# Kernel tuning notes

Hardware: AMD Instinct MI355X
Metric: run time of the kernel (lower is better)

The kernel has to match this reference:

```python
import jax, jax.numpy as jnp
import numpy as np

H = 8        # heads
R = 8        # rank of Lambda
WWIN = 8     # topk window w
T = 2        # num_iterations


def _rotate_half(x):
    h = x.shape[-1] // 2
    return jnp.concatenate([-x[..., h:], x[..., :h]], axis=-1)


def _gelu(x):
    return jax.nn.gelu(x, approximate=False)  # torch nn.GELU default is exact erf


def _forward(target, context, Wt, bt, Wc, bc, Ws1, bs1, Ws2, bs2,
             Wa1, ba1, Wa2, ba2, Wl1, bl1, Wl2, bl2, step_sizes, Wo, bo):
    B, L, D = target.shape
    K = context.shape[1]
    HD = D // H
    u = (target @ Wt + bt).reshape(B, L, H, HD).transpose(0, 2, 1, 3)   # [B,H,L,HD]
    v = (context @ Wc + bc).reshape(B, K, H, HD).transpose(0, 2, 1, 3)  # [B,H,K,HD]

    # scored-window connectivity: first scorer layer is separable over concat([t_i, c_j])
    h1 = (target @ Ws1[:D])[:, :, None, :] + (context @ Ws1[D:])[:, None, :, :] + bs1  # [B,L,K,EH]
    scores = (_gelu(h1) @ Ws2 + bs2)[..., 0]                                           # [B,L,K]
    _, idx = jax.lax.top_k(scores, WWIN)                                               # [B,L,w]
    E = L * WWIN
    edge_j = idx.reshape(B, E)
    edge_i = jnp.broadcast_to(jnp.repeat(jnp.arange(L), WWIN)[None], (B, E))

    # per-edge learnable params R_ij = alpha_ij I + Lambda_ij Lambda_ij^T
    tf = jnp.take_along_axis(target, edge_i[..., None], axis=1)   # [B,E,D]
    cf = jnp.take_along_axis(context, edge_j[..., None], axis=1)  # [B,E,D]
    ef = jnp.concatenate([tf, cf], axis=-1)                       # [B,E,2D]
    alphas = jax.nn.softplus(_gelu(ef @ Wa1 + ba1) @ Wa2 + ba2)[..., 0]     # [B,E]
    Lam = (_gelu(ef @ Wl1 + bl1) @ Wl2 + bl2).reshape(B, E, H, R, HD)
    Lam = Lam / jnp.maximum(jnp.linalg.norm(Lam, axis=-1, keepdims=True), 1e-12)

    # relative-position rotary applied to gathered target states (model_type='SC')
    inv_freq = 1.0 / (10000.0 ** (jnp.arange(0, HD, 2, dtype=jnp.float32) / HD))
    ang = (edge_i - edge_j).astype(jnp.float32)[..., None] * inv_freq       # [B,E,HD/2]
    cos = jnp.concatenate([jnp.cos(ang), jnp.cos(ang)], -1)[:, None]        # [B,1,E,HD]
    sin = jnp.concatenate([jnp.sin(ang), jnp.sin(ang)], -1)[:, None]

    def scatter_edges(res_b, ei_b):  # res_b [H,E,HD] -> [H,L,HD]
        return jax.ops.segment_sum(res_b.transpose(1, 0, 2), ei_b,
                                   num_segments=L).transpose(1, 0, 2)

    for t in range(T):
        step = jax.nn.softplus(step_sizes[t])[None, None, :, None]          # [1,1,L,1] (max_len == L)
        u_i = jnp.take_along_axis(u, edge_i[:, None, :, None], axis=2)      # [B,H,E,HD]
        u_i = u_i * cos + _rotate_half(u_i) * sin
        v_j = jnp.take_along_axis(v, edge_j[:, None, :, None], axis=2)      # [B,H,E,HD]
        diff = u_i - v_j
        Ld = jnp.einsum('behrd,bhed->bher', Lam, diff)                      # [B,H,E,R]
        residual = alphas[:, None, :, None] * diff + jnp.einsum('bher,behrd->bhed', Ld, Lam)
        u = u - step * jax.vmap(scatter_edges)(residual, edge_i)

    y = u.transpose(0, 2, 1, 3).reshape(B, L, D) @ Wo + bo  # dropout is identity in eval
    return y


def setup_inputs() -> dict:
    key = jax.random.key(0)
    B, L, K, D, EH = 2, 2048, 2048, 512, 16
    HD = D // H
    ks = iter(jax.random.split(key, 24))

    def lin(i, o):
        return jax.random.normal(next(ks), (i, o), jnp.float32) * (1.0 / float(np.sqrt(i)))

    def bias(o):
        return jnp.zeros((o,), jnp.float32)

    return {
        'target': jax.random.normal(next(ks), (B, L, D), jnp.float32),
        'context': jax.random.normal(next(ks), (B, K, D), jnp.float32),
        'Wt': lin(D, D), 'bt': bias(D),
        'Wc': lin(D, D), 'bc': bias(D),
        'Ws1': lin(2 * D, EH), 'bs1': bias(EH),
        'Ws2': lin(EH, 1), 'bs2': bias(1),
        'Wa1': lin(2 * D, EH), 'ba1': bias(EH),
        'Wa2': lin(EH, 1), 'ba2': bias(1),
        'Wl1': lin(2 * D, EH), 'bl1': bias(EH),
        'Wl2': lin(EH, H * R * HD), 'bl2': bias(H * R * HD),
        'step_sizes': jnp.full((T, L), -2.2, jnp.float32),
        'Wo': lin(D, D), 'bo': bias(D),
    }


def reference(target, context, Wt, bt, Wc, bc, Ws1, bs1, Ws2, bs2,
              Wa1, ba1, Wa2, ba2, Wl1, bl1, Wl2, bl2, step_sizes, Wo, bo):
    return _forward(target, context, Wt, bt, Wc, bc, Ws1, bs1, Ws2, bs2,
                    Wa1, ba1, Wa2, ba2, Wl1, bl1, Wl2, bl2, step_sizes, Wo, bo)
```

## Files before the change

kernel.cpp:

```cpp
#include <hip/hip_runtime.h>
#include <math.h>

#define BB 2
#define LL 2048
#define KK 2048
#define DD 512
#define HH 8
#define HD_ 64
#define RR 8
#define WWIN 8
#define NE (LL * WWIN)

typedef __attribute__((ext_vector_type(8))) short bf16x8s;
typedef __attribute__((ext_vector_type(4))) float f32x4;

__device__ __forceinline__ float gelu_f(float x) {
    return 0.5f * x * (1.0f + erff(x * 0.70710678118654752f));
}
__device__ __forceinline__ float softplus_f(float x) {
    return (x > 20.0f) ? x : log1pf(expf(x));
}
__device__ __forceinline__ unsigned short f2bf(float f) {
    unsigned int x = __float_as_uint(f);
    x += 0x7FFFu + ((x >> 16) & 1u);
    return (unsigned short)(x >> 16);
}
__device__ __forceinline__ float bf2f(unsigned short s) {
    return __uint_as_float(((unsigned int)s) << 16);
}

__device__ __forceinline__ void gemm_bf16_body(
    const float* __restrict__ A, const float* __restrict__ W,
    const float* __restrict__ bias, float* __restrict__ C,
    int M, int N, int Kd, int bx, int by) {
    __shared__ short As[128][40];
    __shared__ short Bs[64][40];
    const int tid = threadIdx.x;
    const int m0 = bx * 128, n0 = by * 64;
    const int wv = tid >> 6, lane = tid & 63;
    const int wm = (wv & 1) << 6, wn = (wv >> 1) << 5;
    const int l15 = lane & 15, lg = lane >> 4;

    f32x4 acc[4][2] = {};
    union S8 { bf16x8s v; short s[8]; };

    const int arow = tid >> 1, akh = (tid & 1) << 4;
    const int bk = tid >> 3, bnb = (tid & 7) << 3;

    for (int k0 = 0; k0 < Kd; k0 += 32) {
        {
            const float* ap = &A[(size_t)(m0 + arow) * Kd + k0 + akh];
            float4 f0 = *(const float4*)(ap + 0);
            float4 f1 = *(const float4*)(ap + 4);
            float4 f2 = *(const float4*)(ap + 8);
            float4 f3 = *(const float4*)(ap + 12);
            S8 s0, s1;
            s0.s[0] = f2bf(f0.x); s0.s[1] = f2bf(f0.y); s0.s[2] = f2bf(f0.z); s0.s[3] = f2bf(f0.w);
            s0.s[4] = f2bf(f1.x); s0.s[5] = f2bf(f1.y); s0.s[6] = f2bf(f1.z); s0.s[7] = f2bf(f1.w);
            s1.s[0] = f2bf(f2.x); s1.s[1] = f2bf(f2.y); s1.s[2] = f2bf(f2.z); s1.s[3] = f2bf(f2.w);
            s1.s[4] = f2bf(f3.x); s1.s[5] = f2bf(f3.y); s1.s[6] = f2bf(f3.z); s1.s[7] = f2bf(f3.w);
            *(bf16x8s*)&As[arow][akh] = s0.v;
            *(bf16x8s*)&As[arow][akh + 8] = s1.v;
        }
        {
            const float* wp = &W[(size_t)(k0 + bk) * N + n0 + bnb];
            float4 w0 = *(const float4*)(wp + 0);
            float4 w1 = *(const float4*)(wp + 4);
            Bs[bnb + 0][bk] = f2bf(w0.x);
            Bs[bnb + 1][bk] = f2bf(w0.y);
            Bs[bnb + 2][bk] = f2bf(w0.z);
            Bs[bnb + 3][bk] = f2bf(w0.w);
            Bs[bnb + 4][bk] = f2bf(w1.x);
            Bs[bnb + 5][bk] = f2bf(w1.y);
            Bs[bnb + 6][bk] = f2bf(w1.z);
            Bs[bnb + 7][bk] = f2bf(w1.w);
        }
        __syncthreads();
        bf16x8s af[4], bf[2];
#pragma unroll
        for (int mf = 0; mf < 4; ++mf)
            af[mf] = *(const bf16x8s*)&As[wm + (mf << 4) + l15][lg << 3];
#pragma unroll
        for (int nf = 0; nf < 2; ++nf)
            bf[nf] = *(const bf16x8s*)&Bs[wn + (nf << 4) + l15][lg << 3];
#pragma unroll
        for (int mf = 0; mf < 4; ++mf)
#pragma unroll
            for (int nf = 0; nf < 2; ++nf)
                acc[mf][nf] = __builtin_amdgcn_mfma_f32_16x16x32_bf16(af[mf], bf[nf], acc[mf][nf], 0, 0, 0);
        __syncthreads();
    }
    float bv[2] = {0.f, 0.f};
    if (bias) {
        bv[0] = bias[n0 + wn + l15];
        bv[1] = bias[n0 + wn + 16 + l15];
    }
#pragma unroll
    for (int mf = 0; mf < 4; ++mf)
#pragma unroll
        for (int nf = 0; nf < 2; ++nf)
#pragma unroll
            for (int j = 0; j < 4; ++j) {
                int crow = m0 + wm + (mf << 4) + (lg << 2) + j;
                int ccol = n0 + wn + (nf << 4) + l15;
                C[(size_t)crow * N + ccol] = acc[mf][nf][j] + bv[nf];
            }
}

__global__ __launch_bounds__(256) void gemm_bf16(
    const float* __restrict__ A, const float* __restrict__ W,
    const float* __restrict__ bias, float* __restrict__ C,
    int M, int N, int Kd) {
    gemm_bf16_body(A, W, bias, C, M, N, Kd, blockIdx.x, blockIdx.y);
}

__global__ __launch_bounds__(256) void gemm_bf16_dual(
    const float* __restrict__ A0, const float* __restrict__ W0,
    const float* __restrict__ b0, float* __restrict__ C0,
    const float* __restrict__ A1, const float* __restrict__ W1,
    const float* __restrict__ b1, float* __restrict__ C1,
    int M, int N, int Kd) {
    if (blockIdx.z == 0)
        gemm_bf16_body(A0, W0, b0, C0, M, N, Kd, blockIdx.x, blockIdx.y);
    else
        gemm_bf16_body(A1, W1, b1, C1, M, N, Kd, blockIdx.x, blockIdx.y);
}

__device__ __forceinline__ void gemm_f32_body(
    const float* __restrict__ A, const float* __restrict__ W,
    const float* __restrict__ bias, float* __restrict__ C,
    int M, int N, int Kd, int bx, int by) {
    __shared__ float As[16][68];
    __shared__ float Bs[16][68];
    const int tid = threadIdx.x;
    const int m0 = bx * 64, n0 = by * 64;
    const int tx = tid & 15, ty = tid >> 4;
    const int row_a = tid >> 2, kq_a = (tid & 3) << 2;
    const int kw = tid >> 4, nq = (tid & 15) << 2;
    float acc[4][4] = {};
    for (int k0 = 0; k0 < Kd; k0 += 16) {
        float4 av = *(const float4*)&A[(size_t)(m0 + row_a) * Kd + k0 + kq_a];
        As[kq_a + 0][row_a] = av.x;
        As[kq_a + 1][row_a] = av.y;
        As[kq_a + 2][row_a] = av.z;
        As[kq_a + 3][row_a] = av.w;
        *(float4*)&Bs[kw][nq] = *(const float4*)&W[(size_t)(k0 + kw) * N + n0 + nq];
        __syncthreads();
#pragma unroll
        for (int k = 0; k < 16; ++k) {
            float4 a4 = *(const float4*)&As[k][ty << 2];
            float4 b4 = *(const float4*)&Bs[k][tx << 2];
            acc[0][0] = fmaf(a4.x, b4.x, acc[0][0]);
            acc[0][1] = fmaf(a4.x, b4.y, acc[0][1]);
            acc[0][2] = fmaf(a4.x, b4.z, acc[0][2]);
            acc[0][3] = fmaf(a4.x, b4.w, acc[0][3]);
            acc[1][0] = fmaf(a4.y, b4.x, acc[1][0]);
            acc[1][1] = fmaf(a4.y, b4.y, acc[1][1]);
            acc[1][2] = fmaf(a4.y, b4.z, acc[1][2]);
            acc[1][3] = fmaf(a4.y, b4.w, acc[1][3]);
            acc[2][0] = fmaf(a4.z, b4.x, acc[2][0]);
            acc[2][1] = fmaf(a4.z, b4.y, acc[2][1]);
            acc[2][2] = fmaf(a4.z, b4.z, acc[2][2]);
            acc[2][3] = fmaf(a4.z, b4.w, acc[2][3]);
            acc[3][0] = fmaf(a4.w, b4.x, acc[3][0]);
            acc[3][1] = fmaf(a4.w, b4.y, acc[3][1]);
            acc[3][2] = fmaf(a4.w, b4.z, acc[3][2]);
            acc[3][3] = fmaf(a4.w, b4.w, acc[3][3]);
        }
        __syncthreads();
    }
    float4 bv = make_float4(0.f, 0.f, 0.f, 0.f);
    if (bias) bv = *(const float4*)&bias[n0 + (tx << 2)];
#pragma unroll
    for (int q = 0; q < 4; ++q) {
        float4 o;
        o.x = acc[q][0] + bv.x;
        o.y = acc[q][1] + bv.y;
        o.z = acc[q][2] + bv.z;
        o.w = acc[q][3] + bv.w;
        *(float4*)&C[(size_t)(m0 + (ty << 2) + q) * N + n0 + (tx << 2)] = o;
    }
}

__global__ __launch_bounds__(256) void gemm_f32_dual(
    const float* __restrict__ A0, const float* __restrict__ W0, float* __restrict__ C0,
    const float* __restrict__ A1, const float* __restrict__ W1, float* __restrict__ C1,
    int M, int N, int Kd) {
    if (blockIdx.z == 0)
        gemm_f32_body(A0, W0, nullptr, C0, M, N, Kd, blockIdx.x, blockIdx.y);
    else
        gemm_f32_body(A1, W1, nullptr, C1, M, N, Kd, blockIdx.x, blockIdx.y);
}

__global__ void prep_wcat(const float* __restrict__ Ws1, const float* __restrict__ Wa1,
                          const float* __restrict__ Wl1,
                          const float* __restrict__ Wl2, const float* __restrict__ bl2,
                          float* __restrict__ Wct, float* __restrict__ Wcc,
                          unsigned short* __restrict__ wl2bfT) {
    if (blockIdx.x < 128) {
        int idx = blockIdx.x * 256 + threadIdx.x;
        int k = idx >> 6, c = idx & 63;
        float vt = 0.f, vc = 0.f;
        if (c < 16)      { vt = Ws1[k * 16 + c];        vc = Ws1[(512 + k) * 16 + c]; }
        else if (c < 32) { vt = Wa1[k * 16 + (c - 16)]; vc = Wa1[(512 + k) * 16 + (c - 16)]; }
        else if (c < 48) { vt = Wl1[k * 16 + (c - 32)]; vc = Wl1[(512 + k) * 16 + (c - 32)]; }
        Wct[idx] = vt;
        Wcc[idx] = vc;
    } else {
        int c = (blockIdx.x - 128) * 256 + threadIdx.x;
        union U8 { bf16x8s v; unsigned short s[8]; } r0, r1, r2, r3;
#pragma unroll
        for (int k = 0; k < 8; ++k) r0.s[k] = f2bf(Wl2[(size_t)k * 4096 + c]);
#pragma unroll
        for (int k = 0; k < 8; ++k) r1.s[k] = f2bf(Wl2[(size_t)(k + 8) * 4096 + c]);
#pragma unroll
        for (int k = 0; k < 8; ++k) { r2.s[k] = 0; r3.s[k] = 0; }
        r2.s[0] = f2bf(bl2[c]);
        unsigned short* dst = &wl2bfT[(size_t)c * 32];
        *(bf16x8s*)(dst + 0)  = r0.v;
        *(bf16x8s*)(dst + 8)  = r1.v;
        *(bf16x8s*)(dst + 16) = r2.v;
        *(bf16x8s*)(dst + 24) = r3.v;
    }
}

__global__ __launch_bounds__(256) void scores_topk(
    const float* __restrict__ t64, const float* __restrict__ c64,
    const float* __restrict__ bs1, const float* __restrict__ Ws2,
    const float* __restrict__ bs2, int* __restrict__ edge_j) {
    __shared__ float sc[KK];
    __shared__ float rs[256];
    __shared__ int ri[256];
    const int tid = threadIdx.x;
    const int b = blockIdx.x >> 11;
    const int i = blockIdx.x & (LL - 1);
    float tsb[16], w2[16];
    const float* tr = &t64[(size_t)(b * LL + i) * 64];
#pragma unroll
    for (int k = 0; k < 16; ++k) { tsb[k] = tr[k] + bs1[k]; w2[k] = Ws2[k]; }
    const float b2 = bs2[0];
    for (int j = tid; j < KK; j += 256) {
        const float4* cr4 = (const float4*)&c64[(size_t)(b * KK + j) * 64];
        float creg[16];
        float4 c0 = cr4[0], c1 = cr4[1], c2 = cr4[2], c3 = cr4[3];
        creg[0] = c0.x; creg[1] = c0.y; creg[2] = c0.z; creg[3] = c0.w;
        creg[4] = c1.x; creg[5] = c1.y; creg[6] = c1.z; creg[7] = c1.w;
        creg[8] = c2.x; creg[9] = c2.y; creg[10] = c2.z; creg[11] = c2.w;
        creg[12] = c3.x; creg[13] = c3.y; creg[14] = c3.z; creg[15] = c3.w;
        float s = b2;
#pragma unroll
        for (int k = 0; k < 16; ++k)
            s = fmaf(gelu_f(tsb[k] + creg[k]), w2[k], s);
        sc[j] = s;
    }
    __syncthreads();
    for (int w = 0; w < WWIN; ++w) {
        float bs_ = -INFINITY;
        int bi_ = KK;
        for (int j = tid; j < KK; j += 256) {
            float s = sc[j];
            if (s > bs_) { bs_ = s; bi_ = j; }
        }
        rs[tid] = bs_;
        ri[tid] = bi_;
        __syncthreads();
        for (int off = 128; off > 0; off >>= 1) {
            if (tid < off) {
                float so = rs[tid + off];
                int io = ri[tid + off];
                if (so > rs[tid] || (so == rs[tid] && io < ri[tid])) { rs[tid] = so; ri[tid] = io; }
            }
            __syncthreads();
        }
        if (tid == 0) {
            int bj = ri[0];
            edge_j[(size_t)(b * LL + i) * WWIN + w] = bj;
            sc[bj] = -INFINITY;
        }
        __syncthreads();
    }
}

__global__ __launch_bounds__(256) void edge_params(
    const float* __restrict__ t64, const float* __restrict__ c64,
    const int* __restrict__ edge_j,
    const float* __restrict__ bl1, const float* __restrict__ ba1,
    const float* __restrict__ Wa2, const float* __restrict__ ba2,
    unsigned short* __restrict__ h16bf, float* __restrict__ alpha) {
    int idx = blockIdx.x * 256 + threadIdx.x;
    if (idx >= BB * NE) return;
    int b = idx >> 14;
    int i = (idx & (NE - 1)) >> 3;
    int j = edge_j[idx];
    const float* tr = &t64[(size_t)(b * LL + i) * 64];
    const float* cr = &c64[(size_t)(b * KK + j) * 64];
    union U8 { bf16x8s v; unsigned short s[8]; } o0, o1, o2, o3;
    float s = ba2[0];
#pragma unroll
    for (int k = 0; k < 8; ++k) {
        o0.s[k] = f2bf(gelu_f(tr[32 + k] + cr[32 + k] + bl1[k]));
        s = fmaf(gelu_f(tr[16 + k] + cr[16 + k] + ba1[k]), Wa2[k], s);
    }
#pragma unroll
    for (int k = 8; k < 16; ++k) {
        o1.s[k - 8] = f2bf(gelu_f(tr[32 + k] + cr[32 + k] + bl1[k]));
        s = fmaf(gelu_f(tr[16 + k] + cr[16 + k] + ba1[k]), Wa2[k], s);
    }
#pragma unroll
    for (int k = 0; k < 8; ++k) { o2.s[k] = 0; o3.s[k] = 0; }
    o2.s[0] = 0x3F80;
    unsigned short* dst = &h16bf[(size_t)idx * 32];
    *(bf16x8s*)(dst + 0)  = o0.v;
    *(bf16x8s*)(dst + 8)  = o1.v;
    *(bf16x8s*)(dst + 16) = o2.v;
    *(bf16x8s*)(dst + 24) = o3.v;
    alpha[idx] = softplus_f(s);
}

__global__ __launch_bounds__(256, 3) void iterate_k(
    float* __restrict__ u, const float* __restrict__ v,
    const int* __restrict__ edge_j, const float* __restrict__ alpha,
    const unsigned short* __restrict__ h16bf,
    const unsigned short* __restrict__ wl2bfT,
    const float* __restrict__ step_sizes) {
    __shared__ unsigned short lam_s[32 * 520];
    __shared__ float alphs[32];
    __shared__ int ejs[32];
    __shared__ float dts[4][64];
    const int tid = threadIdx.x;
    const int h = blockIdx.y, b = blockIdx.z;
    const int i0 = blockIdx.x << 2;
    const int e0 = b * NE + (i0 << 3);

    if (tid < 32) { ejs[tid] = edge_j[e0 + tid]; alphs[tid] = alpha[e0 + tid]; }

    const int wv = tid >> 6, lane = tid & 63;
    const int l15 = lane & 15, lg = lane >> 4;

    {
        const int mt = wv & 1;
        const int ncol0 = (wv >> 1) << 8;
        bf16x8s afrag = *(const bf16x8s*)&h16bf[(size_t)(e0 + (mt << 4) + l15) * 32 + (lg << 3)];
        const unsigned short* wrow = &wl2bfT[((size_t)(h * 512 + ncol0 + l15)) * 32 + (lg << 3)];
#pragma unroll
        for (int nt = 0; nt < 16; ++nt) {
            bf16x8s bfrag = *(const bf16x8s*)(wrow + nt * 512);
            f32x4 acc = {0.f, 0.f, 0.f, 0.f};
            acc = __builtin_amdgcn_mfma_f32_16x16x32_bf16(afrag, bfrag, acc, 0, 0, 0);
            const int col = ncol0 + (nt << 4) + l15;
            const int d = col & 63, r = col >> 6;
#pragma unroll
            for (int j = 0; j < 4; ++j) {
                const int e = (mt << 4) + (lg << 2) + j;
                lam_s[e * 520 + (d << 3) + r] = f2bf(acc[j]);
            }
        }
    }
    __syncthreads();

    const int i = i0 + wv;
    const size_t urow = ((size_t)(b * LL + i)) * DD + h * HD_ + lane;
    float u_d = u[urow];
    const float st0 = softplus_f(step_sizes[i]);
    const float st1 = softplus_f(step_sizes[LL + i]);

    const bool up32 = (lane & 32) != 0;
    const bool up16 = (lane & 16) != 0;
    const bool up8  = (lane & 8) != 0;
    const bool up4  = (lane & 4) != 0;
    const bool up2  = (lane & 2) != 0;
    const bool up1  = (lane & 1) != 0;

    float lamr[8][8];
#pragma unroll
    for (int w = 0; w < 8; ++w) {
        union U8 { bf16x8s v; unsigned short s[8]; } lv;
        lv.v = *(const bf16x8s*)&lam_s[((wv << 3) + w) * 520 + (lane << 3)];
#pragma unroll
        for (int r = 0; r < 8; ++r) lamr[w][r] = bf2f(lv.s[r]);
    }

    float inv_ss;
    {
        float q[32];
#pragma unroll
        for (int wp = 0; wp < 4; ++wp)
#pragma unroll
            for (int r = 0; r < 8; ++r) {
                float plo = lamr[wp][r] * lamr[wp][r];
                float phi = lamr[wp + 4][r] * lamr[wp + 4][r];
                float recv = __shfl_xor(up32 ? plo : phi, 32);
                q[(wp << 3) + r] = (up32 ? phi : plo) + recv;
            }
#pragma unroll
        for (int j = 0; j < 16; ++j) {
            float lo = q[j], hi = q[j + 16];
            float recv = __shfl_xor(up16 ? lo : hi, 16);
            q[j] = (up16 ? hi : lo) + recv;
        }
#pragma unroll
        for (int j = 0; j < 8; ++j) {
            float lo = q[j], hi = q[j + 8];
            float recv = __shfl_xor(up8 ? lo : hi, 8);
            q[j] = (up8 ? hi : lo) + recv;
        }
#pragma unroll
        for (int j = 0; j < 4; ++j) {
            float lo = q[j], hi = q[j + 4];
            float recv = __shfl_xor(up4 ? lo : hi, 4);
            q[j] = (up4 ? hi : lo) + recv;
        }
#pragma unroll
        for (int j = 0; j < 2; ++j) {
            float lo = q[j], hi = q[j + 2];
            float recv = __shfl_xor(up2 ? lo : hi, 2);
            q[j] = (up2 ? hi : lo) + recv;
        }
        {
            float lo = q[0], hi = q[1];
            float recv = __shfl_xor(up1 ? lo : hi, 1);
            q[0] = (up1 ? hi : lo) + recv;
        }
        inv_ss = 1.0f / fmaxf(q[0], 1e-24f);
    }

    const int k31 = lane & 31;
    const float invf = exp2f((float)k31 * (-13.287712379549449f / 32.0f));
    float vw[8], cw[8], sw[8], aw[8];
#pragma unroll
    for (int w = 0; w < 8; ++w) {
        const int le = (wv << 3) + w;
        const int j = ejs[le];
        aw[w] = alphs[le];
        vw[w] = v[((size_t)(b * KK + j)) * DD + h * HD_ + lane];
        float ang = (float)(i - j) * invf;
        sincosf(ang, &sw[w], &cw[w]);
    }

#pragma unroll
    for (int t = 0; t < 2; ++t) {
        float upv = __shfl_xor(u_d, 32);
        float rotb = (lane < 32) ? -upv : upv;
        float resid = 0.0f;
        float q[32];
#pragma unroll
        for (int wp = 0; wp < 4; ++wp) {
            float dlo = fmaf(u_d, cw[wp], rotb * sw[wp]) - vw[wp];
            float dhi = fmaf(u_d, cw[wp + 4], rotb * sw[wp + 4]) - vw[wp + 4];
            resid = fmaf(aw[wp], dlo, resid);
            resid = fmaf(aw[wp + 4], dhi, resid);
#pragma unroll
            for (int r = 0; r < 8; ++r) {
                float plo = lamr[wp][r] * dlo;
                float phi = lamr[wp + 4][r] * dhi;
                float recv = __shfl_xor(up32 ? plo : phi, 32);
                q[(wp << 3) + r] = (up32 ? phi : plo) + recv;
            }
        }
#pragma unroll
        for (int j = 0; j < 16; ++j) {
            float lo = q[j], hi = q[j + 16];
            float recv = __shfl_xor(up16 ? lo : hi, 16);
            q[j] = (up16 ? hi : lo) + recv;
        }
#pragma unroll
        for (int j = 0; j < 8; ++j) {
            float lo = q[j], hi = q[j + 8];
            float recv = __shfl_xor(up8 ? lo : hi, 8);
            q[j] = (up8 ? hi : lo) + recv;
        }
#pragma unroll
        for (int j = 0; j < 4; ++j) {
            float lo = q[j], hi = q[j + 4];
            float recv = __shfl_xor(up4 ? lo : hi, 4);
            q[j] = (up4 ? hi : lo) + recv;
        }
#pragma unroll
        for (int j = 0; j < 2; ++j) {
            float lo = q[j], hi = q[j + 2];
            float recv = __shfl_xor(up2 ? lo : hi, 2);
            q[j] = (up2 ? hi : lo) + recv;
        }
        {
            float lo = q[0], hi = q[1];
            float recv = __shfl_xor(up1 ? lo : hi, 1);
            q[0] = (up1 ? hi : lo) + recv;
        }
        dts[wv][lane] = q[0] * inv_ss;
#pragma unroll
        for (int w = 0; w < 8; ++w) {
            float4 da = *(const float4*)&dts[wv][(w << 3)];
            float4 db = *(const float4*)&dts[wv][(w << 3) + 4];
            resid = fmaf(da.x, lamr[w][0], resid);
            resid = fmaf(da.y, lamr[w][1], resid);
            resid = fmaf(da.z, lamr[w][2], resid);
            resid = fmaf(da.w, lamr[w][3], resid);
            resid = fmaf(db.x, lamr[w][4], resid);
            resid = fmaf(db.y, lamr[w][5], resid);
            resid = fmaf(db.z, lamr[w][6], resid);
            resid = fmaf(db.w, lamr[w][7], resid);
        }
        u_d = fmaf((t == 0) ? -st0 : -st1, resid, u_d);
    }
    u[urow] = u_d;
}

extern "C" void kernel_launch(void* const* d_in, const int* in_sizes, int n_in,
                              void* d_out, int out_size, void* d_ws, size_t ws_size,
                              hipStream_t stream) {
    (void)in_sizes; (void)n_in; (void)out_size; (void)ws_size;
    const float* target     = (const float*)d_in[0];
    const float* context    = (const float*)d_in[1];
    const float* Wt         = (const float*)d_in[2];
    const float* bt         = (const float*)d_in[3];
    const float* Wc         = (const float*)d_in[4];
    const float* bc         = (const float*)d_in[5];
    const float* Ws1        = (const float*)d_in[6];
    const float* bs1        = (const float*)d_in[7];
    const float* Ws2        = (const float*)d_in[8];
    const float* bs2        = (const float*)d_in[9];
    const float* Wa1        = (const float*)d_in[10];
    const float* ba1        = (const float*)d_in[11];
    const float* Wa2        = (const float*)d_in[12];
    const float* ba2        = (const float*)d_in[13];
    const float* Wl1        = (const float*)d_in[14];
    const float* bl1        = (const float*)d_in[15];
    const float* Wl2        = (const float*)d_in[16];
    const float* bl2        = (const float*)d_in[17];
    const float* step_sizes = (const float*)d_in[18];
    const float* Wo         = (const float*)d_in[19];
    const float* bo         = (const float*)d_in[20];
    float* out = (float*)d_out;

    float* ws = (float*)d_ws;
    float* u    = ws;
    float* v    = ws + 2097152;
    float* t64  = ws + 4194304;
    float* c64  = ws + 4456448;
    unsigned short* h16bf = (unsigned short*)(ws + 4718592);
    float* alph = ws + 5242880;
    int*   ej   = (int*)(ws + 5275648);
    float* wct  = ws + 5308416;
    float* wcc  = ws + 5341184;
    unsigned short* wl2bfT = (unsigned short*)(ws + 5373952);

    prep_wcat<<<dim3(144), dim3(256), 0, stream>>>(Ws1, Wa1, Wl1, Wl2, bl2, wct, wcc, wl2bfT);

    gemm_bf16_dual<<<dim3(32, 8, 2), dim3(256), 0, stream>>>(
        target, Wt, bt, u, context, Wc, bc, v, 4096, 512, 512);

    gemm_f32_dual<<<dim3(64, 1, 2), dim3(256), 0, stream>>>(
        target, wct, t64, context, wcc, c64, 4096, 64, 512);

    scores_topk<<<dim3(BB * LL), dim3(256), 0, stream>>>(t64, c64, bs1, Ws2, bs2, ej);

    edge_params<<<dim3(BB * NE / 256), dim3(256), 0, stream>>>(t64, c64, ej, bl1, ba1, Wa2, ba2, h16bf, alph);

    iterate_k<<<dim3(LL / 4, HH, BB), dim3(256), 0, stream>>>(u, v, ej, alph, h16bf, wl2bfT, step_sizes);

    gemm_bf16<<<dim3(32, 8), dim3(256), 0, stream>>>(u, Wo, bo, out, 4096, 512, 512);
}
```

Before: 313.6 us.

## Register-resident top-k with wave shuffles, packed Lambda stores, precomputed rotary table

scores_topk now keeps each thread's 8 scores in registers, sorts them with a small sorting network, and picks each winner with a wave-level shuffle reduction plus a 4-entry cross-wave merge. This replaces the shared-memory score array and the barrier-heavy tree reduction that ran once per window slot. iterate_k restructures its MFMA loop so each lane computes four rank columns for the same d. It packs them into a single 64-bit LDS store instead of scattered 16-bit writes. A new rot_prep kernel builds a cos/sin table indexed by relative offset into the now-unused t64 buffer, so iterate_k replaces its per-edge sincosf with a table lookup, at the cost of an extra launch and more global reads.

```diff
diff --git a/kernel.cpp b/kernel.cpp
--- a/kernel.cpp
+++ b/kernel.cpp
@@ -224,13 +224,22 @@
     }
 }
 
+__global__ __launch_bounds__(256) void rot_prep(float* __restrict__ rot) {
+    int idx = blockIdx.x * 256 + threadIdx.x;
+    int dlt = (idx >> 5) - 2047;
+    int k = idx & 31;
+    float invf = exp2f((float)k * (-13.287712379549449f / 32.0f));
+    float s, c;
+    sincosf((float)dlt * invf, &s, &c);
+    ((float2*)rot)[idx] = make_float2(c, s);
+}
+
 __global__ __launch_bounds__(256) void scores_topk(
     const float* __restrict__ t64, const float* __restrict__ c64,
     const float* __restrict__ bs1, const float* __restrict__ Ws2,
     const float* __restrict__ bs2, int* __restrict__ edge_j) {
-    __shared__ float sc[KK];
-    __shared__ float rs[256];
-    __shared__ int ri[256];
+    __shared__ float wvs[4];
+    __shared__ int wvj[4];
     const int tid = threadIdx.x;
     const int b = blockIdx.x >> 11;
     const int i = blockIdx.x & (LL - 1);
@@ -239,7 +248,12 @@
 #pragma unroll
     for (int k = 0; k < 16; ++k) { tsb[k] = tr[k] + bs1[k]; w2[k] = Ws2[k]; }
     const float b2 = bs2[0];
-    for (int j = tid; j < KK; j += 256) {
+
+    float ls[8];
+    int lj[8];
+#pragma unroll
+    for (int k8 = 0; k8 < 8; ++k8) {
+        const int j = tid + (k8 << 8);
         const float4* cr4 = (const float4*)&c64[(size_t)(b * KK + j) * 64];
         float creg[16];
         float4 c0 = cr4[0], c1 = cr4[1], c2 = cr4[2], c3 = cr4[3];
@@ -251,31 +265,51 @@
 #pragma unroll
         for (int k = 0; k < 16; ++k)
             s = fmaf(gelu_f(tsb[k] + creg[k]), w2[k], s);
-        sc[j] = s;
-    }
-    __syncthreads();
+        ls[k8] = s;
+        lj[k8] = j;
+    }
+
+#define CSWAP(X, Y) do { \
+        float ax = ls[X], ay = ls[Y]; int jx = lj[X], jy = lj[Y]; \
+        bool sw = (ay > ax) || (ay == ax && jy < jx); \
+        ls[X] = sw ? ay : ax; ls[Y] = sw ? ax : ay; \
+        lj[X] = sw ? jy : jx; lj[Y] = sw ? jx : jy; \
+    } while (0)
+    CSWAP(0, 1); CSWAP(2, 3); CSWAP(4, 5); CSWAP(6, 7);
+    CSWAP(0, 2); CSWAP(1, 3); CSWAP(4, 6); CSWAP(5, 7);
+    CSWAP(1, 2); CSWAP(5, 6);
+    CSWAP(0, 4); CSWAP(1, 5); CSWAP(2, 6); CSWAP(3, 7);
+    CSWAP(2, 4); CSWAP(3, 5);
+    CSWAP(1, 2); CSWAP(3, 4); CSWAP(5, 6);
+#undef CSWAP
+
+    const int lane = tid & 63, wv = tid >> 6;
+#pragma unroll
     for (int w = 0; w < WWIN; ++w) {
-        float bs_ = -INFINITY;
-        int bi_ = KK;
-        for (int j = tid; j < KK; j += 256) {
-            float s = sc[j];
-            if (s > bs_) { bs_ = s; bi_ = j; }
-        }
-        rs[tid] = bs_;
-        ri[tid] = bi_;
+        float cs = ls[0];
+        int cj = lj[0];
+#pragma unroll
+        for (int m = 1; m < 64; m <<= 1) {
+            float os = __shfl_xor(cs, m);
+            int oj = __shfl_xor(cj, m);
+            if (os > cs || (os == cs && oj < cj)) { cs = os; cj = oj; }
+        }
+        if (lane == 0) { wvs[wv] = cs; wvj[wv] = cj; }
         __syncthreads();
-        for (int off = 128; off > 0; off >>= 1) {
-            if (tid < off) {
-                float so = rs[tid + off];
-                int io = ri[tid + off];
-                if (so > rs[tid] || (so == rs[tid] && io < ri[tid])) { rs[tid] = so; ri[tid] = io; }
-            }
-            __syncthreads();
-        }
-        if (tid == 0) {
-            int bj = ri[0];
-            edge_j[(size_t)(b * LL + i) * WWIN + w] = bj;
-            sc[bj] = -INFINITY;
+        float bsv = wvs[0];
+        int bjv = wvj[0];
+#pragma unroll
+        for (int q = 1; q < 4; ++q) {
+            float qs = wvs[q];
+            int qj = wvj[q];
+            if (qs > bsv || (qs == bsv && qj < bjv)) { bsv = qs; bjv = qj; }
+        }
+        if (tid == 0) edge_j[(size_t)(b * LL + i) * WWIN + w] = bjv;
+        if (lj[0] == bjv) {
+#pragma unroll
+            for (int k = 0; k < 7; ++k) { ls[k] = ls[k + 1]; lj[k] = lj[k + 1]; }
+            ls[7] = -INFINITY;
+            lj[7] = 0x7fffffff;
         }
         __syncthreads();
     }
@@ -322,6 +356,7 @@
     const int* __restrict__ edge_j, const float* __restrict__ alpha,
     const unsigned short* __restrict__ h16bf,
     const unsigned short* __restrict__ wl2bfT,
+    const float* __restrict__ rotT,
     const float* __restrict__ step_sizes) {
     __shared__ unsigned short lam_s[32 * 520];
     __shared__ float alphs[32];
@@ -339,20 +374,25 @@
 
     {
         const int mt = wv & 1;
-        const int ncol0 = (wv >> 1) << 8;
+        const int rbase = (wv >> 1) << 2;
         bf16x8s afrag = *(const bf16x8s*)&h16bf[(size_t)(e0 + (mt << 4) + l15) * 32 + (lg << 3)];
-        const unsigned short* wrow = &wl2bfT[((size_t)(h * 512 + ncol0 + l15)) * 32 + (lg << 3)];
-#pragma unroll
-        for (int nt = 0; nt < 16; ++nt) {
-            bf16x8s bfrag = *(const bf16x8s*)(wrow + nt * 512);
-            f32x4 acc = {0.f, 0.f, 0.f, 0.f};
-            acc = __builtin_amdgcn_mfma_f32_16x16x32_bf16(afrag, bfrag, acc, 0, 0, 0);
-            const int col = ncol0 + (nt << 4) + l15;
-            const int d = col & 63, r = col >> 6;
+        const unsigned short* wbase = &wl2bfT[((size_t)(h * 512 + (rbase << 6) + l15)) * 32 + (lg << 3)];
+#pragma unroll
+        for (int g = 0; g < 4; ++g) {
+            f32x4 a0 = {0.f, 0.f, 0.f, 0.f}, a1 = a0, a2 = a0, a3 = a0;
+            const unsigned short* wg = wbase + g * 512;
+            a0 = __builtin_amdgcn_mfma_f32_16x16x32_bf16(afrag, *(const bf16x8s*)(wg + 0),    a0, 0, 0, 0);
+            a1 = __builtin_amdgcn_mfma_f32_16x16x32_bf16(afrag, *(const bf16x8s*)(wg + 2048), a1, 0, 0, 0);
+            a2 = __builtin_amdgcn_mfma_f32_16x16x32_bf16(afrag, *(const bf16x8s*)(wg + 4096), a2, 0, 0, 0);
+            a3 = __builtin_amdgcn_mfma_f32_16x16x32_bf16(afrag, *(const bf16x8s*)(wg + 6144), a3, 0, 0, 0);
+            const int d = (g << 4) + l15;
 #pragma unroll
             for (int j = 0; j < 4; ++j) {
                 const int e = (mt << 4) + (lg << 2) + j;
-                lam_s[e * 520 + (d << 3) + r] = f2bf(acc[j]);
+                uint2 pk;
+                pk.x = (unsigned int)f2bf(a0[j]) | ((unsigned int)f2bf(a1[j]) << 16);
+                pk.y = (unsigned int)f2bf(a2[j]) | ((unsigned int)f2bf(a3[j]) << 16);
+                *(uint2*)&lam_s[e * 520 + (d << 3) + rbase] = pk;
             }
         }
     }
@@ -425,7 +465,6 @@
     }
 
     const int k31 = lane & 31;
-    const float invf = exp2f((float)k31 * (-13.287712379549449f / 32.0f));
     float vw[8], cw[8], sw[8], aw[8];
 #pragma unroll
     for (int w = 0; w < 8; ++w) {
@@ -433,8 +472,9 @@
         const int j = ejs[le];
         aw[w] = alphs[le];
         vw[w] = v[((size_t)(b * KK + j)) * DD + h * HD_ + lane];
-        float ang = (float)(i - j) * invf;
-        sincosf(ang, &sw[w], &cw[w]);
+        float2 rc = ((const float2*)rotT)[((size_t)(i - j + 2047) << 5) + k31];
+        cw[w] = rc.x;
+        sw[w] = rc.y;
     }
 
 #pragma unroll
@@ -543,6 +583,7 @@
     float* wct  = ws + 5308416;
     float* wcc  = ws + 5341184;
     unsigned short* wl2bfT = (unsigned short*)(ws + 5373952);
+    float* rotT = t64;
 
     prep_wcat<<<dim3(144), dim3(256), 0, stream>>>(Ws1, Wa1, Wl1, Wl2, bl2, wct, wcc, wl2bfT);
 
@@ -556,7 +597,9 @@
 
     edge_params<<<dim3(BB * NE / 256), dim3(256), 0, stream>>>(t64, c64, ej, bl1, ba1, Wa2, ba2, h16bf, alph);
 
-    iterate_k<<<dim3(LL / 4, HH, BB), dim3(256), 0, stream>>>(u, v, ej, alph, h16bf, wl2bfT, step_sizes);
+    rot_prep<<<dim3(512), dim3(256), 0, stream>>>(rotT);
+
+    iterate_k<<<dim3(LL / 4, HH, BB), dim3(256), 0, stream>>>(u, v, ej, alph, h16bf, wl2bfT, rotT, step_sizes);
 
     gemm_bf16<<<dim3(32, 8), dim3(256), 0, stream>>>(u, Wo, bo, out, 4096, 512, 512);
 }
```

Result: slower. 595.7 us (+90.0%).
